# Optimization experiments

Hardware: AMD Instinct MI355X
Metric: run time of the kernel (lower is better)

## Reference

```python
import jax, jax.numpy as jnp
import numpy as np

B, N, D = 8, 512, 1024
E, H, TOP_K = 8, 8, 2
HD = D // H
EPS = 1e-5


def setup_inputs() -> dict:
    key = jax.random.key(0)
    ks = jax.random.split(key, 8)
    # kaiming_uniform with a=sqrt(5) over fan_in=N -> bound = sqrt(6/((1+5)*N)) = 1/sqrt(N)
    bound_w = 1.0 / np.sqrt(N)
    bound_lin = 1.0 / np.sqrt(D)
    return {
        "x": jax.random.normal(ks[0], (B, N, D), dtype=jnp.float32),
        "weight": jax.random.uniform(ks[1], (E, H, N, N), jnp.float32, -bound_w, bound_w),
        "bias": jnp.zeros((E, H, N), jnp.float32),
        "router_w": jax.random.uniform(ks[2], (E, D), jnp.float32, -bound_lin, bound_lin),
        "in_w": jax.random.uniform(ks[3], (D, D), jnp.float32, -bound_lin, bound_lin),
        "in_b": jax.random.uniform(ks[4], (D,), jnp.float32, -bound_lin, bound_lin),
        "out_w": jax.random.uniform(ks[5], (D, D), jnp.float32, -bound_lin, bound_lin),
        "out_b": jax.random.uniform(ks[6], (D,), jnp.float32, -bound_lin, bound_lin),
    }


def reference(x, weight, bias, router_w, in_w, in_b, out_w, out_b):
    # Router: mean-pool tokens, linear, softmax, top-k
    router_logits = x.mean(axis=1) @ router_w.T              # (B, E)
    router_probs = jax.nn.softmax(router_logits, axis=-1)
    top_w, top_i = jax.lax.top_k(router_probs, TOP_K)        # (B, K)
    top_w = top_w / top_w.sum(axis=-1, keepdims=True)

    # Input projection -> (B, H, hd, N), layer-norm over token axis N (no affine)
    xp = x @ in_w.T + in_b                                   # (B, N, D)
    xr = xp.reshape(B, N, H, HD).transpose(0, 2, 3, 1)       # (B, H, hd, N)
    mu = xr.mean(axis=-1, keepdims=True)
    var = xr.var(axis=-1, keepdims=True)
    xn = (xr - mu) * jax.lax.rsqrt(var + EPS)

    # Gather per-(batch, head, k) NxN expert matrices, row-softmax
    w = weight[top_i].transpose(0, 2, 1, 3, 4)               # (B, H, K, N, N)
    b = bias[top_i].transpose(0, 2, 1, 3)                    # (B, H, K, N)
    w_attn = jax.nn.softmax(w, axis=-1)

    # out[b,h,k,d,m] = sum_n xn[b,h,d,n] * w_attn[b,h,k,m,n]
    out = jnp.einsum('bhdn,bhkmn->bhkdm', xn, w_attn)
    out = out + b[:, :, :, None, :]                          # (B, H, K, hd, N)
    out = (out * top_w[:, None, :, None, None]).sum(axis=2)  # (B, H, hd, N)

    out = out.transpose(0, 3, 1, 2).reshape(B, N, D)         # (B, N, D)
    out = out @ out_w.T + out_b

    # Load-balancing aux loss
    top1 = top_i[:, 0]
    expert_mask = jax.nn.one_hot(top1, E, dtype=jnp.float32)
    aux = E * (router_probs.mean(axis=0) * expert_mask.mean(axis=0)).sum()
    return out, aux
```

## Files before the change

### kernel.cpp

```cpp
#include <hip/hip_runtime.h>
#include <hip/hip_bf16.h>

#define Bv 8
#define Nv 512
#define Dv 1024
#define Ev 8
#define Hv 8
#define HDv 128
#define EPSv 1e-5f

typedef __attribute__((ext_vector_type(8))) short short8;
typedef __attribute__((ext_vector_type(4))) float f32x4;

__device__ __forceinline__ unsigned short f2b(float f) {
    __hip_bfloat16 h = __float2bfloat16(f);
    return *reinterpret_cast<unsigned short*>(&h);
}
__device__ __forceinline__ float bf2f(unsigned int u) {
    union { unsigned int i; float f; } v; v.i = u << 16; return v.f;
}

__device__ __forceinline__ void gld16(const void* g, void* l) {
    __builtin_amdgcn_global_load_lds(
        (const __attribute__((address_space(1))) void*)(uintptr_t)(g),
        (__attribute__((address_space(3))) void*)(uintptr_t)(l), 16, 0, 0);
}

__global__ __launch_bounds__(256) void k_preA(const float* __restrict__ x,
                                              const float* __restrict__ w1,
                                              const float* __restrict__ w2,
                                              unsigned short* __restrict__ xb,
                                              float* __restrict__ part_x,
                                              unsigned short* __restrict__ w1b,
                                              unsigned short* __restrict__ w2b) {
    int bid = blockIdx.x;
    int t = threadIdx.x;
    if (bid < 128) {
        int b = bid >> 4, c = bid & 15;
        const float* px = x + ((size_t)b * Nv + c * 32) * Dv + t * 4;
        unsigned short* qx = xb + ((size_t)b * Nv + c * 32) * Dv + t * 4;
        float4 s4 = make_float4(0.f, 0.f, 0.f, 0.f);
        #pragma unroll 8
        for (int r = 0; r < 32; ++r) {
            float4 v = *(const float4*)(px + (size_t)r * Dv);
            s4.x += v.x; s4.y += v.y; s4.z += v.z; s4.w += v.w;
            uint2 pk;
            pk.x = (unsigned)f2b(v.x) | ((unsigned)f2b(v.y) << 16);
            pk.y = (unsigned)f2b(v.z) | ((unsigned)f2b(v.w) << 16);
            *(uint2*)(qx + (size_t)r * Dv) = pk;
        }
        *(float4*)(part_x + ((size_t)(b * 16 + c)) * Dv + t * 4) = s4;
        return;
    }
    const float* src; unsigned short* dst; int base;
    if (bid < 256) { src = w1; dst = w1b; base = (bid - 128) * 8192; }
    else           { src = w2; dst = w2b; base = (bid - 256) * 8192; }
    #pragma unroll
    for (int i = 0; i < 8; ++i) {
        float4 a = *(const float4*)(src + base + i * 1024 + t * 4);
        uint2 p;
        p.x = (unsigned)f2b(a.x) | ((unsigned)f2b(a.y) << 16);
        p.y = (unsigned)f2b(a.z) | ((unsigned)f2b(a.w) << 16);
        *(uint2*)(dst + base + i * 1024 + t * 4) = p;
    }
}

template <int MODE>
__global__ __launch_bounds__(256) void k_gemm(
    const unsigned short* __restrict__ A,
    const unsigned short* __restrict__ W,
    const float* __restrict__ bias,
    void* __restrict__ Cv,
    float2* __restrict__ part,
    const float* __restrict__ part_x,
    float* __restrict__ xmean,
    int M, int Nn, int K) {
    __shared__ __align__(16) unsigned short sA[3][128 * 64];
    __shared__ __align__(16) unsigned short sB[3][128 * 64];
    const int t = threadIdx.x;
    const int bn = blockIdx.x * 128;
    const int bm = blockIdx.y * 128;
    const int lane = t & 63;
    const int w = t >> 6, wm = w >> 1, wn = w & 1;
    const int fr = lane & 15, fq = lane >> 4;
    const int NT = K >> 6;
    f32x4 acc[4][4] = {};

#define STAGE(s, k0)                                                        \
    {                                                                       \
        _Pragma("unroll")                                                   \
        for (int i_ = 0; i_ < 4; ++i_) {                                    \
            int c_ = t + i_ * 256;                                          \
            int row_ = c_ >> 3, col_ = c_ & 7;                              \
            int cs_ = col_ ^ (row_ & 7);                                    \
            gld16(A + (size_t)(bm + row_) * K + (k0) + cs_ * 8, &sA[s][c_ * 8]); \
            gld16(W + (size_t)(bn + row_) * K + (k0) + cs_ * 8, &sB[s][c_ * 8]); \
        }                                                                   \
    }

    STAGE(0, 0);
    STAGE(1, 64);
    if (MODE == 2) {
        int blk = blockIdx.y * 8 + blockIdx.x;
        int o = blk * 32 + (t >> 3);
        int c2 = t & 7;
        int b2 = o >> 10, d2 = o & 1023;
        float S = part_x[((size_t)(b2 * 16 + c2)) * Dv + d2]
                + part_x[((size_t)(b2 * 16 + c2 + 8)) * Dv + d2];
        S += __shfl_xor(S, 1); S += __shfl_xor(S, 2); S += __shfl_xor(S, 4);
        if (c2 == 0) xmean[o] = S * (1.f / Nv);
    }
    for (int it = 0; it < NT; ++it) {
        if (it + 2 < NT) {
            STAGE((it + 2) % 3, (it + 2) * 64);
            asm volatile("s_waitcnt vmcnt(16)" ::: "memory");
        } else if (it + 1 < NT) {
            asm volatile("s_waitcnt vmcnt(8)" ::: "memory");
        } else {
            asm volatile("s_waitcnt vmcnt(0)" ::: "memory");
        }
        __builtin_amdgcn_s_barrier();
        const unsigned short* pA = sA[it % 3];
        const unsigned short* pB = sB[it % 3];
        #pragma unroll
        for (int kk = 0; kk < 2; ++kk) {
            short8 af[4], bv[4];
            #pragma unroll
            for (int i = 0; i < 4; ++i)
                af[i] = *(const short8*)&pA[(wm * 64 + i * 16 + fr) * 64 + (((kk << 2) + fq) ^ (fr & 7)) * 8];
            #pragma unroll
            for (int j = 0; j < 4; ++j)
                bv[j] = *(const short8*)&pB[(wn * 64 + j * 16 + fr) * 64 + (((kk << 2) + fq) ^ (fr & 7)) * 8];
            #pragma unroll
            for (int i = 0; i < 4; ++i)
                #pragma unroll
                for (int j = 0; j < 4; ++j)
                    acc[i][j] = __builtin_amdgcn_mfma_f32_16x16x32_bf16(af[i], bv[j], acc[i][j], 0, 0, 0);
        }
        __builtin_amdgcn_s_barrier();
    }
#undef STAGE
    if (MODE == 0) {
        #pragma unroll
        for (int j = 0; j < 4; ++j) {
            const int n = bn + wn * 64 + j * 16 + fr;
            const float bj = bias[n];
            #pragma unroll
            for (int i = 0; i < 4; ++i) {
                const int m0 = bm + wm * 64 + i * 16 + fq * 4;
                #pragma unroll
                for (int r = 0; r < 4; ++r)
                    ((float*)Cv)[(size_t)(m0 + r) * Nn + n] = acc[i][j][r] + bj;
            }
        }
    } else {
        unsigned short* sc = &sA[0][0];
        float2* red = (float2*)&sB[0][0];
        const int bB   = bm >> 9;
        const int tok0 = bm & 511;
        const int chunk = (bm >> 7) & 3;
        #pragma unroll
        for (int j = 0; j < 4; ++j) {
            const int col = wn * 64 + j * 16 + fr;
            const float bj = bias[bn + col];
            float s = 0.f, q = 0.f;
            #pragma unroll
            for (int i = 0; i < 4; ++i) {
                const int row0 = wm * 64 + i * 16 + fq * 4;
                #pragma unroll
                for (int r = 0; r < 4; r += 2) {
                    float v0 = acc[i][j][r] + bj;
                    float v1 = acc[i][j][r + 1] + bj;
                    s += v0 + v1;
                    q = fmaf(v0, v0, fmaf(v1, v1, q));
                    unsigned int pk = (unsigned int)f2b(v0) | ((unsigned int)f2b(v1) << 16);
                    *(unsigned int*)&sc[col * 136 + row0 + r] = pk;
                }
            }
            red[col * 8 + wm * 4 + fq] = make_float2(s, q);
        }
        __syncthreads();
        if (t < 128) {
            float S = 0.f, Q = 0.f;
            #pragma unroll
            for (int k = 0; k < 8; ++k) { float2 v = red[t * 8 + k]; S += v.x; Q += v.y; }
            part[((size_t)bB * Dv + bn + t) * 4 + chunk] = make_float2(S, Q);
        }
        unsigned short* dst = (unsigned short*)Cv;
        #pragma unroll
        for (int k = 0; k < 8; ++k) {
            const int c = t + k * 256;
            const int dl = c >> 4, tk = c & 15;
            uint4 v = *(const uint4*)&sc[dl * 136 + tk * 8];
            *(uint4*)&dst[((size_t)bB * Dv + bn + dl) * Nv + tok0 + tk * 8] = v;
        }
    }
}

__global__ __launch_bounds__(256) void k_mixg(
    const float* __restrict__ weight,
    const unsigned short* __restrict__ xpT,
    const float* __restrict__ bias,
    const float* __restrict__ xmean,
    const float* __restrict__ router_w,
    const float2* __restrict__ part,
    unsigned short* __restrict__ y,
    float* __restrict__ aux_out) {
    __shared__ __align__(16) unsigned short sA[2][128 * 64];
    __shared__ __align__(16) unsigned short sB[2][128 * 64];
    __shared__ float probs[Bv][Ev];
    __shared__ float twsh[Bv][2];
    __shared__ int   tsel[Bv][2];
    __shared__ int   top1s[Bv];
    const int t = threadIdx.x;
    const int bm = blockIdx.x * 128;
    const int bh = blockIdx.y;
    const int b = bh >> 3, h = bh & 7;

    {
        int pid = t >> 2, l = t & 3;
        int rb = pid >> 3, re = pid & 7;
        const float4* xm = (const float4*)(xmean + rb * Dv);
        const float4* rw = (const float4*)(router_w + re * Dv);
        float s = 0.f;
        #pragma unroll
        for (int j = 0; j < 64; ++j) {
            float4 aa = xm[l + j * 4], ww = rw[l + j * 4];
            s = fmaf(aa.x, ww.x, s); s = fmaf(aa.y, ww.y, s);
            s = fmaf(aa.z, ww.z, s); s = fmaf(aa.w, ww.w, s);
        }
        s += __shfl_xor(s, 1); s += __shfl_xor(s, 2);
        if (l == 0) probs[rb][re] = s;
    }
    __syncthreads();
    if (t < Bv) {
        int bb = t;
        float mx = -1e30f;
        for (int e2 = 0; e2 < Ev; ++e2) mx = fmaxf(mx, probs[bb][e2]);
        float sum = 0.f;
        for (int e2 = 0; e2 < Ev; ++e2) { float v = __expf(probs[bb][e2] - mx); probs[bb][e2] = v; sum += v; }
        float inv = 1.f / sum;
        for (int e2 = 0; e2 < Ev; ++e2) probs[bb][e2] *= inv;
        int i0 = 0; float p0 = probs[bb][0];
        for (int e2 = 1; e2 < Ev; ++e2) if (probs[bb][e2] > p0) { p0 = probs[bb][e2]; i0 = e2; }
        int i1 = -1; float p1 = -1.f;
        for (int e2 = 0; e2 < Ev; ++e2) if (e2 != i0 && probs[bb][e2] > p1) { p1 = probs[bb][e2]; i1 = e2; }
        float s2 = p0 + p1;
        tsel[bb][0] = i0; tsel[bb][1] = i1;
        twsh[bb][0] = p0 / s2; twsh[bb][1] = p1 / s2;
        top1s[bb] = i0;
    }
    __syncthreads();
    if (blockIdx.x == 0 && bh == 0 && t == 0) {
        float aux = 0.f;
        for (int e2 = 0; e2 < Ev; ++e2) {
            float pm = 0.f, mm = 0.f;
            for (int bb = 0; bb < Bv; ++bb) { pm += probs[bb][e2]; mm += (top1s[bb] == e2) ? 1.f : 0.f; }
            aux += (pm / Bv) * (mm / Bv);
        }
        *aux_out = aux * Ev;
    }
    const int e0 = tsel[b][0], e1 = tsel[b][1];
    const float tw0 = twsh[b][0], tw1 = twsh[b][1];

    const int lane = t & 63;
    const int w = t >> 6, wm = w >> 1, wn = w & 1;
    const int fr = lane & 15, fq = lane >> 4;

    float rstd_j[4], nmr_j[4];
    #pragma unroll
    for (int j = 0; j < 4; ++j) {
        const int dg = h * HDv + wn * 64 + j * 16 + fr;
        const float2* pp = part + ((size_t)b * Dv + dg) * 4;
        float S = 0.f, Q = 0.f;
        #pragma unroll
        for (int cc = 0; cc < 4; ++cc) { float2 v = pp[cc]; S += v.x; Q += v.y; }
        float mu = S * (1.f / Nv);
        float var = Q * (1.f / Nv) - mu * mu;
        float rs = rsqrtf(var + EPSv);
        rstd_j[j] = rs; nmr_j[j] = -mu * rs;
    }

    const float* W0 = weight + (size_t)(e0 * Hv + h) * Nv * Nv;
    const float* W1 = weight + (size_t)(e1 * Hv + h) * Nv * Nv;
    const unsigned short* Bb = xpT + ((size_t)b * Dv + h * HDv) * Nv;

    float c0s[4], c1s[4];
    {
        float s0a[4] = {0.f, 0.f, 0.f, 0.f}, s1a[4] = {0.f, 0.f, 0.f, 0.f};
        for (int k0 = 0; k0 < Nv; k0 += 64) {
            #pragma unroll
            for (int i = 0; i < 4; ++i) {
                int c = t + i * 256;
                int row = c >> 3, col = c & 7;
                int cs = col ^ (row & 7);
                size_t off = (size_t)(bm + row) * Nv + k0 + cs * 8;
                float4 a0 = *(const float4*)&W0[off];
                float4 a1 = *(const float4*)&W0[off + 4];
                float4 b0 = *(const float4*)&W1[off];
                float4 b1 = *(const float4*)&W1[off + 4];
                s0a[i] += ((__expf(a0.x) + __expf(a0.y)) + (__expf(a0.z) + __expf(a0.w)))
                        + ((__expf(a1.x) + __expf(a1.y)) + (__expf(a1.z) + __expf(a1.w)));
                s1a[i] += ((__expf(b0.x) + __expf(b0.y)) + (__expf(b0.z) + __expf(b0.w)))
                        + ((__expf(b1.x) + __expf(b1.y)) + (__expf(b1.z) + __expf(b1.w)));
            }
        }
        #pragma unroll
        for (int i = 0; i < 4; ++i) {
            #pragma unroll
            for (int off = 1; off < 8; off <<= 1) {
                s0a[i] += __shfl_xor(s0a[i], off);
                s1a[i] += __shfl_xor(s1a[i], off);
            }
            c0s[i] = tw0 / s0a[i];
            c1s[i] = tw1 / s1a[i];
        }
    }

    const int NT = Nv >> 6;
    f32x4 acc[4][4] = {};
    float4 ra0[4][2], ra1[4][2];

#define BSTAGE(s, k0)                                                       \
    {                                                                       \
        _Pragma("unroll")                                                   \
        for (int i_ = 0; i_ < 4; ++i_) {                                    \
            int c_ = t + i_ * 256;                                          \
            int row_ = c_ >> 3, col_ = c_ & 7;                              \
            int cs_ = col_ ^ (row_ & 7);                                    \
            gld16(Bb + (size_t)row_ * Nv + (k0) + cs_ * 8, &sB[s][c_ * 8]); \
        }                                                                   \
    }
#define ALOAD(k0)                                                           \
    {                                                                       \
        _Pragma("unroll")                                                   \
        for (int i_ = 0; i_ < 4; ++i_) {                                    \
            int c_ = t + i_ * 256;                                          \
            int row_ = c_ >> 3, col_ = c_ & 7;                              \
            int cs_ = col_ ^ (row_ & 7);                                    \
            size_t off_ = (size_t)(bm + row_) * Nv + (k0) + cs_ * 8;        \
            ra0[i_][0] = *(const float4*)&W0[off_];                         \
            ra0[i_][1] = *(const float4*)&W0[off_ + 4];                     \
            ra1[i_][0] = *(const float4*)&W1[off_];                         \
            ra1[i_][1] = *(const float4*)&W1[off_ + 4];                     \
        }                                                                   \
    }

    BSTAGE(0, 0);
    ALOAD(0);
    for (int it = 0; it < NT; ++it) {
        if (it + 1 < NT) {
            BSTAGE((it + 1) & 1, (it + 1) * 64);
            asm volatile("s_waitcnt vmcnt(4)" ::: "memory");
        } else {
            asm volatile("s_waitcnt vmcnt(0)" ::: "memory");
        }
        #pragma unroll
        for (int i = 0; i < 4; ++i) {
            int c = t + i * 256;
            float o[8];
            const float4 a0 = ra0[i][0], a1 = ra0[i][1];
            const float4 b0 = ra1[i][0], b1 = ra1[i][1];
            o[0] = c0s[i] * __expf(a0.x) + c1s[i] * __expf(b0.x);
            o[1] = c0s[i] * __expf(a0.y) + c1s[i] * __expf(b0.y);
            o[2] = c0s[i] * __expf(a0.z) + c1s[i] * __expf(b0.z);
            o[3] = c0s[i] * __expf(a0.w) + c1s[i] * __expf(b0.w);
            o[4] = c0s[i] * __expf(a1.x) + c1s[i] * __expf(b1.x);
            o[5] = c0s[i] * __expf(a1.y) + c1s[i] * __expf(b1.y);
            o[6] = c0s[i] * __expf(a1.z) + c1s[i] * __expf(b1.z);
            o[7] = c0s[i] * __expf(a1.w) + c1s[i] * __expf(b1.w);
            uint4 pk;
            pk.x = (unsigned)f2b(o[0]) | ((unsigned)f2b(o[1]) << 16);
            pk.y = (unsigned)f2b(o[2]) | ((unsigned)f2b(o[3]) << 16);
            pk.z = (unsigned)f2b(o[4]) | ((unsigned)f2b(o[5]) << 16);
            pk.w = (unsigned)f2b(o[6]) | ((unsigned)f2b(o[7]) << 16);
            *(uint4*)&sA[it & 1][c * 8] = pk;
        }
        if (it + 1 < NT) ALOAD((it + 1) * 64);
        asm volatile("s_waitcnt lgkmcnt(0)" ::: "memory");
        __builtin_amdgcn_s_barrier();
        const unsigned short* pA = sA[it & 1];
        const unsigned short* pB = sB[it & 1];
        #pragma unroll
        for (int kk = 0; kk < 2; ++kk) {
            short8 af[4], bv[4];
            #pragma unroll
            for (int i = 0; i < 4; ++i)
                af[i] = *(const short8*)&pA[(wm * 64 + i * 16 + fr) * 64 + (((kk << 2) + fq) ^ (fr & 7)) * 8];
            #pragma unroll
            for (int j = 0; j < 4; ++j)
                bv[j] = *(const short8*)&pB[(wn * 64 + j * 16 + fr) * 64 + (((kk << 2) + fq) ^ (fr & 7)) * 8];
            #pragma unroll
            for (int i = 0; i < 4; ++i)
                #pragma unroll
                for (int j = 0; j < 4; ++j)
                    acc[i][j] = __builtin_amdgcn_mfma_f32_16x16x32_bf16(af[i], bv[j], acc[i][j], 0, 0, 0);
        }
        __builtin_amdgcn_s_barrier();
    }
#undef BSTAGE
#undef ALOAD
    #pragma unroll
    for (int i = 0; i < 4; ++i) {
        #pragma unroll
        for (int r = 0; r < 4; ++r) {
            const int m = bm + wm * 64 + i * 16 + fq * 4 + r;
            const float br = tw0 * bias[(size_t)(e0 * Hv + h) * Nv + m]
                           + tw1 * bias[(size_t)(e1 * Hv + h) * Nv + m];
            #pragma unroll
            for (int j = 0; j < 4; ++j) {
                const int d = wn * 64 + j * 16 + fr;
                float v = fmaf(acc[i][j][r], rstd_j[j], nmr_j[j] + br);
                y[((size_t)b * Nv + m) * Dv + h * HDv + d] = f2b(v);
            }
        }
    }
}

extern "C" void kernel_launch(void* const* d_in, const int* in_sizes, int n_in,
                              void* d_out, int out_size, void* d_ws, size_t ws_size,
                              hipStream_t stream) {
    const float* x        = (const float*)d_in[0];
    const float* weight   = (const float*)d_in[1];
    const float* bias     = (const float*)d_in[2];
    const float* router_w = (const float*)d_in[3];
    const float* in_w     = (const float*)d_in[4];
    const float* in_b     = (const float*)d_in[5];
    const float* out_w    = (const float*)d_in[6];
    const float* out_b    = (const float*)d_in[7];
    float* out = (float*)d_out;

    if (ws_size < ((size_t)63 << 20)) return;

    char* wsb = (char*)d_ws;
    float*  xmean  = (float*)(wsb);
    float2* part   = (float2*)(wsb + (64 << 10));
    float*  part_x = (float*)(wsb + (512 << 10));
    unsigned short* in_wb  = (unsigned short*)(wsb + ((size_t)2 << 20));
    unsigned short* out_wb = (unsigned short*)(wsb + ((size_t)4 << 20));
    unsigned short* xb     = (unsigned short*)(wsb + ((size_t)8 << 20));
    unsigned short* xpT    = (unsigned short*)(wsb + ((size_t)16 << 20));
    unsigned short* y = xb;

    k_preA<<<384, 256, 0, stream>>>(x, in_w, out_w, xb, part_x, in_wb, out_wb);
    k_gemm<2><<<dim3(8, 32), 256, 0, stream>>>(xb, in_wb, in_b, xpT, part, part_x, xmean,
                                               Bv * Nv, Dv, Dv);
    k_mixg<<<dim3(4, 64), 256, 0, stream>>>(weight, xpT, bias, xmean, router_w, part, y,
                                            out + (size_t)Bv * Nv * Dv);
    k_gemm<0><<<dim3(8, 32), 256, 0, stream>>>(y, out_wb, out_b, out, nullptr, nullptr, nullptr,
                                               Bv * Nv, Dv, Dv);
}
```

Baseline: 76.78 us.

## Defer softmax normalization to epilogue, running separate MFMA accumulators per expert

Drops the separate pre-pass that read both expert weight tiles to compute row softmax denominators. Unnormalized exp values for each expert are now staged into their own LDS buffer and multiplied in separate accumulators, with row sums gathered during the main loop and the per-row scale applied in the epilogue. This halves reads of the large fp32 weight tensor and removes the duplicate exp work. In exchange it doubles MFMA count, LDS footprint for A and accumulator registers, which may lower occupancy.

```diff
diff --git a/kernel.cpp b/kernel.cpp
--- a/kernel.cpp
+++ b/kernel.cpp
@@ -206,8 +206,10 @@
     const float2* __restrict__ part,
     unsigned short* __restrict__ y,
     float* __restrict__ aux_out) {
-    __shared__ __align__(16) unsigned short sA[2][128 * 64];
+    __shared__ __align__(16) unsigned short sA0[2][128 * 64];
+    __shared__ __align__(16) unsigned short sA1[2][128 * 64];
     __shared__ __align__(16) unsigned short sB[2][128 * 64];
+    __shared__ float rowc0[128], rowc1[128];
     __shared__ float probs[Bv][Ev];
     __shared__ float twsh[Bv][2];
     __shared__ int   tsel[Bv][2];
@@ -285,41 +287,10 @@
     const float* W1 = weight + (size_t)(e1 * Hv + h) * Nv * Nv;
     const unsigned short* Bb = xpT + ((size_t)b * Dv + h * HDv) * Nv;
 
-    float c0s[4], c1s[4];
-    {
-        float s0a[4] = {0.f, 0.f, 0.f, 0.f}, s1a[4] = {0.f, 0.f, 0.f, 0.f};
-        for (int k0 = 0; k0 < Nv; k0 += 64) {
-            #pragma unroll
-            for (int i = 0; i < 4; ++i) {
-                int c = t + i * 256;
-                int row = c >> 3, col = c & 7;
-                int cs = col ^ (row & 7);
-                size_t off = (size_t)(bm + row) * Nv + k0 + cs * 8;
-                float4 a0 = *(const float4*)&W0[off];
-                float4 a1 = *(const float4*)&W0[off + 4];
-                float4 b0 = *(const float4*)&W1[off];
-                float4 b1 = *(const float4*)&W1[off + 4];
-                s0a[i] += ((__expf(a0.x) + __expf(a0.y)) + (__expf(a0.z) + __expf(a0.w)))
-                        + ((__expf(a1.x) + __expf(a1.y)) + (__expf(a1.z) + __expf(a1.w)));
-                s1a[i] += ((__expf(b0.x) + __expf(b0.y)) + (__expf(b0.z) + __expf(b0.w)))
-                        + ((__expf(b1.x) + __expf(b1.y)) + (__expf(b1.z) + __expf(b1.w)));
-            }
-        }
-        #pragma unroll
-        for (int i = 0; i < 4; ++i) {
-            #pragma unroll
-            for (int off = 1; off < 8; off <<= 1) {
-                s0a[i] += __shfl_xor(s0a[i], off);
-                s1a[i] += __shfl_xor(s1a[i], off);
-            }
-            c0s[i] = tw0 / s0a[i];
-            c1s[i] = tw1 / s1a[i];
-        }
-    }
-
     const int NT = Nv >> 6;
-    f32x4 acc[4][4] = {};
+    f32x4 acc0[4][4] = {}, acc1[4][4] = {};
     float4 ra0[4][2], ra1[4][2];
+    float s0p[4] = {0.f, 0.f, 0.f, 0.f}, s1p[4] = {0.f, 0.f, 0.f, 0.f};
 
 #define BSTAGE(s, k0)                                                       \
     {                                                                       \
@@ -358,59 +329,92 @@
         #pragma unroll
         for (int i = 0; i < 4; ++i) {
             int c = t + i * 256;
-            float o[8];
+            float e0v[8], e1v[8];
             const float4 a0 = ra0[i][0], a1 = ra0[i][1];
             const float4 b0 = ra1[i][0], b1 = ra1[i][1];
-            o[0] = c0s[i] * __expf(a0.x) + c1s[i] * __expf(b0.x);
-            o[1] = c0s[i] * __expf(a0.y) + c1s[i] * __expf(b0.y);
-            o[2] = c0s[i] * __expf(a0.z) + c1s[i] * __expf(b0.z);
-            o[3] = c0s[i] * __expf(a0.w) + c1s[i] * __expf(b0.w);
-            o[4] = c0s[i] * __expf(a1.x) + c1s[i] * __expf(b1.x);
-            o[5] = c0s[i] * __expf(a1.y) + c1s[i] * __expf(b1.y);
-            o[6] = c0s[i] * __expf(a1.z) + c1s[i] * __expf(b1.z);
-            o[7] = c0s[i] * __expf(a1.w) + c1s[i] * __expf(b1.w);
-            uint4 pk;
-            pk.x = (unsigned)f2b(o[0]) | ((unsigned)f2b(o[1]) << 16);
-            pk.y = (unsigned)f2b(o[2]) | ((unsigned)f2b(o[3]) << 16);
-            pk.z = (unsigned)f2b(o[4]) | ((unsigned)f2b(o[5]) << 16);
-            pk.w = (unsigned)f2b(o[6]) | ((unsigned)f2b(o[7]) << 16);
-            *(uint4*)&sA[it & 1][c * 8] = pk;
+            e0v[0] = __expf(a0.x); e0v[1] = __expf(a0.y);
+            e0v[2] = __expf(a0.z); e0v[3] = __expf(a0.w);
+            e0v[4] = __expf(a1.x); e0v[5] = __expf(a1.y);
+            e0v[6] = __expf(a1.z); e0v[7] = __expf(a1.w);
+            e1v[0] = __expf(b0.x); e1v[1] = __expf(b0.y);
+            e1v[2] = __expf(b0.z); e1v[3] = __expf(b0.w);
+            e1v[4] = __expf(b1.x); e1v[5] = __expf(b1.y);
+            e1v[6] = __expf(b1.z); e1v[7] = __expf(b1.w);
+            s0p[i] += ((e0v[0] + e0v[1]) + (e0v[2] + e0v[3]))
+                    + ((e0v[4] + e0v[5]) + (e0v[6] + e0v[7]));
+            s1p[i] += ((e1v[0] + e1v[1]) + (e1v[2] + e1v[3]))
+                    + ((e1v[4] + e1v[5]) + (e1v[6] + e1v[7]));
+            uint4 p0, p1;
+            p0.x = (unsigned)f2b(e0v[0]) | ((unsigned)f2b(e0v[1]) << 16);
+            p0.y = (unsigned)f2b(e0v[2]) | ((unsigned)f2b(e0v[3]) << 16);
+            p0.z = (unsigned)f2b(e0v[4]) | ((unsigned)f2b(e0v[5]) << 16);
+            p0.w = (unsigned)f2b(e0v[6]) | ((unsigned)f2b(e0v[7]) << 16);
+            p1.x = (unsigned)f2b(e1v[0]) | ((unsigned)f2b(e1v[1]) << 16);
+            p1.y = (unsigned)f2b(e1v[2]) | ((unsigned)f2b(e1v[3]) << 16);
+            p1.z = (unsigned)f2b(e1v[4]) | ((unsigned)f2b(e1v[5]) << 16);
+            p1.w = (unsigned)f2b(e1v[6]) | ((unsigned)f2b(e1v[7]) << 16);
+            *(uint4*)&sA0[it & 1][c * 8] = p0;
+            *(uint4*)&sA1[it & 1][c * 8] = p1;
         }
         if (it + 1 < NT) ALOAD((it + 1) * 64);
         asm volatile("s_waitcnt lgkmcnt(0)" ::: "memory");
         __builtin_amdgcn_s_barrier();
-        const unsigned short* pA = sA[it & 1];
+        const unsigned short* pA0 = sA0[it & 1];
+        const unsigned short* pA1 = sA1[it & 1];
         const unsigned short* pB = sB[it & 1];
         #pragma unroll
         for (int kk = 0; kk < 2; ++kk) {
-            short8 af[4], bv[4];
-            #pragma unroll
-            for (int i = 0; i < 4; ++i)
-                af[i] = *(const short8*)&pA[(wm * 64 + i * 16 + fr) * 64 + (((kk << 2) + fq) ^ (fr & 7)) * 8];
+            short8 bv[4];
             #pragma unroll
             for (int j = 0; j < 4; ++j)
                 bv[j] = *(const short8*)&pB[(wn * 64 + j * 16 + fr) * 64 + (((kk << 2) + fq) ^ (fr & 7)) * 8];
             #pragma unroll
-            for (int i = 0; i < 4; ++i)
+            for (int i = 0; i < 4; ++i) {
+                const int aoff = (wm * 64 + i * 16 + fr) * 64 + (((kk << 2) + fq) ^ (fr & 7)) * 8;
+                short8 af0 = *(const short8*)&pA0[aoff];
+                short8 af1 = *(const short8*)&pA1[aoff];
                 #pragma unroll
                 for (int j = 0; j < 4; ++j)
-                    acc[i][j] = __builtin_amdgcn_mfma_f32_16x16x32_bf16(af[i], bv[j], acc[i][j], 0, 0, 0);
+                    acc0[i][j] = __builtin_amdgcn_mfma_f32_16x16x32_bf16(af0, bv[j], acc0[i][j], 0, 0, 0);
+                #pragma unroll
+                for (int j = 0; j < 4; ++j)
+                    acc1[i][j] = __builtin_amdgcn_mfma_f32_16x16x32_bf16(af1, bv[j], acc1[i][j], 0, 0, 0);
+            }
         }
         __builtin_amdgcn_s_barrier();
     }
 #undef BSTAGE
 #undef ALOAD
+
     #pragma unroll
     for (int i = 0; i < 4; ++i) {
         #pragma unroll
+        for (int off = 1; off < 8; off <<= 1) {
+            s0p[i] += __shfl_xor(s0p[i], off);
+            s1p[i] += __shfl_xor(s1p[i], off);
+        }
+        int row = (t >> 3) + i * 32;
+        if ((t & 7) == 0) {
+            rowc0[row] = tw0 / s0p[i];
+            rowc1[row] = tw1 / s1p[i];
+        }
+    }
+    __syncthreads();
+
+    #pragma unroll
+    for (int i = 0; i < 4; ++i) {
+        #pragma unroll
         for (int r = 0; r < 4; ++r) {
-            const int m = bm + wm * 64 + i * 16 + fq * 4 + r;
+            const int ml = wm * 64 + i * 16 + fq * 4 + r;
+            const int m = bm + ml;
+            const float c0m = rowc0[ml], c1m = rowc1[ml];
             const float br = tw0 * bias[(size_t)(e0 * Hv + h) * Nv + m]
                            + tw1 * bias[(size_t)(e1 * Hv + h) * Nv + m];
             #pragma unroll
             for (int j = 0; j < 4; ++j) {
                 const int d = wn * 64 + j * 16 + fr;
-                float v = fmaf(acc[i][j][r], rstd_j[j], nmr_j[j] + br);
+                float vb = c0m * acc0[i][j][r] + c1m * acc1[i][j][r];
+                float v = fmaf(vb, rstd_j[j], nmr_j[j] + br);
                 y[((size_t)b * Nv + m) * Dv + h * HDv + d] = f2b(v);
             }
         }
```

Result: faster. 73.86 us, median of 2 (-3.8%).
